# Performance work log

Hardware: AMD Instinct MI355X
Metric: run time of the kernel (lower is better)

Reference implementation:

```python
import jax, jax.numpy as jnp
import numpy as np

E = 1024      # embed_dim
H = 16        # num_heads
DH = E // H   # head_dim
CD = 512      # context_dim
S = 2048      # source length
B = 16        # batch
SCALE = DH ** -0.5


def setup_inputs() -> dict:
    key0 = jax.random.key(0)
    ks = jax.random.split(key0, 12)
    inp = {
        "query": jax.random.normal(ks[0], (1, B, E), jnp.float32),
        "key": jax.random.normal(ks[1], (S, B, E), jnp.float32),
        "value": jax.random.normal(ks[2], (S, B, E), jnp.float32),
        "context": jax.random.normal(ks[3], (B, CD), jnp.float32),
        # packed QKV input projection: [3E, E] (rows 0:E -> Q, E:2E -> K, 2E:3E -> V)
        "in_proj_weight": jax.random.normal(ks[4], (3 * E, E), jnp.float32) * 0.02,
        "in_proj_bias": jnp.zeros((3 * E,), jnp.float32),
        # context_layer: Linear(context_dim + embed_dim, embed_dim)
        "ctx_weight": jax.random.normal(ks[5], (E, CD + E), jnp.float32) * 0.02,
        "ctx_bias": jnp.zeros((E,), jnp.float32),
        # out_proj: Linear(E, E)
        "out_weight": jax.random.normal(ks[6], (E, E), jnp.float32) * 0.02,
        "out_bias": jnp.zeros((E,), jnp.float32),
        # bias_k / bias_v: learned extra KV position, shape [1,1,E] in torch
        "bias_k": jax.random.normal(ks[7], (E,), jnp.float32) * 0.02,
        "bias_v": jax.random.normal(ks[8], (E,), jnp.float32) * 0.02,
    }
    return inp


def _attention(query, key, value, context, in_proj_weight, in_proj_bias,
               ctx_weight, ctx_bias, out_weight, out_bias, bias_k, bias_v):
    tgt_len, bsz, _ = query.shape  # tgt_len == 1 (context cat requires it)
    # separate q/k/v input projections (slices of packed weight)
    q = query @ in_proj_weight[:E].T + in_proj_bias[:E]
    k = key @ in_proj_weight[E:2 * E].T + in_proj_bias[E:2 * E]
    v = value @ in_proj_weight[2 * E:].T + in_proj_bias[2 * E:]
    # context injection: concat context along feature dim, project back to E
    ctx_q = context[None]                                # [1, B, CD]
    ctx_k = jnp.broadcast_to(context[None], (k.shape[0], bsz, CD))
    q = jnp.concatenate([ctx_q, q], axis=-1) @ ctx_weight.T + ctx_bias
    k = jnp.concatenate([ctx_k, k], axis=-1) @ ctx_weight.T + ctx_bias
    q = q * SCALE
    # bias_k / bias_v appended as extra source position
    k = jnp.concatenate([k, jnp.broadcast_to(bias_k, (1, bsz, E))], axis=0)
    v = jnp.concatenate([v, jnp.broadcast_to(bias_v, (1, bsz, E))], axis=0)
    src_len = k.shape[0]
    # [L, B, E] -> [B*H, L, DH]
    qh = q.reshape(tgt_len, bsz * H, DH).transpose(1, 0, 2)
    kh = k.reshape(src_len, bsz * H, DH).transpose(1, 0, 2)
    vh = v.reshape(src_len, bsz * H, DH).transpose(1, 0, 2)
    scores = jnp.einsum("btd,bsd->bts", qh, kh)          # [B*H, T, S+1]
    weights = jax.nn.softmax(scores, axis=-1)
    attn = jnp.einsum("bts,bsd->btd", weights, vh)       # [B*H, T, DH]
    attn = attn.transpose(1, 0, 2).reshape(tgt_len, bsz, E)
    attn = attn @ out_weight.T + out_bias
    avg_weights = weights.reshape(bsz, H, tgt_len, src_len).sum(axis=1) / H
    return attn, avg_weights


def reference(query, key, value, context, in_proj_weight, in_proj_bias,
              ctx_weight, ctx_bias, out_weight, out_bias, bias_k, bias_v):
    return _attention(query, key, value, context, in_proj_weight, in_proj_bias,
                      ctx_weight, ctx_bias, out_weight, out_bias, bias_k, bias_v)
```

## Files before the change

### kernel.cpp

```cpp
#include <hip/hip_runtime.h>
#include <math.h>

#define E   1024
#define H   16
#define DH  64
#define CD  512
#define S   2048
#define B   16
#define SRC (S + 1)
#define SPAD 2052
#define SCALE 0.125f

#define OFF_CTXP 0
#define OFF_Q0   16384
#define OFF_BKP  32768
#define OFF_Q1S  33792
#define OFF_CK   50176
#define OFF_TT   66560
#define OFF_GP   328960
#define OFF_SC   1377536
#define OFF_WT   1902848
#define OFF_UP   2427392
#define OFF_U    10816000
#define OFF_AP   11078144

__global__ __launch_bounds__(256) void k_pre1(
    const float* __restrict__ query, const float* __restrict__ context,
    const float* __restrict__ ipw, const float* __restrict__ ipb,
    const float* __restrict__ cw, const float* __restrict__ cb,
    float* __restrict__ ws)
{
    int b  = blockIdx.x >> 6;
    int et = blockIdx.x & 63;
    int grp = threadIdx.x >> 4, l = threadIdx.x & 15;
    int e = et * 16 + grp;
    const float* crow = cw + (size_t)e * (CD + E);
    const float* ctx  = context + b * CD;
    float a1 = 0.f;
    #pragma unroll
    for (int c = l * 4; c < CD; c += 64) {
        float4 w4 = *(const float4*)(crow + c);
        float4 x4 = *(const float4*)(ctx + c);
        a1 += w4.x*x4.x + w4.y*x4.y + w4.z*x4.z + w4.w*x4.w;
    }
    const float* qrow = query + b * E;
    const float* wrow = ipw + (size_t)e * E;
    float a2 = 0.f;
    #pragma unroll
    for (int f = l * 4; f < E; f += 64) {
        float4 w4 = *(const float4*)(wrow + f);
        float4 x4 = *(const float4*)(qrow + f);
        a2 += w4.x*x4.x + w4.y*x4.y + w4.z*x4.z + w4.w*x4.w;
    }
    float a3 = 0.f;
    if (b == 0) {
        const float* c2 = crow + CD;
        const float* bk = ipb + E;
        #pragma unroll
        for (int f = l * 4; f < E; f += 64) {
            float4 w4 = *(const float4*)(c2 + f);
            float4 x4 = *(const float4*)(bk + f);
            a3 += w4.x*x4.x + w4.y*x4.y + w4.z*x4.z + w4.w*x4.w;
        }
    }
    #pragma unroll
    for (int m = 8; m >= 1; m >>= 1) {
        a1 += __shfl_xor(a1, m, 64);
        a2 += __shfl_xor(a2, m, 64);
        a3 += __shfl_xor(a3, m, 64);
    }
    if (l == 0) {
        ws[OFF_CTXP + b*E + e] = a1 + cb[e];
        ws[OFF_Q0   + b*E + e] = a2 + ipb[e];
        if (b == 0) ws[OFF_BKP + e] = a3;
    }
}

__global__ __launch_bounds__(256) void k_pre2(
    const float* __restrict__ cw, float* __restrict__ ws)
{
    int b  = blockIdx.x >> 6;
    int et = blockIdx.x & 63;
    int grp = threadIdx.x >> 4, l = threadIdx.x & 15;
    int e = et * 16 + grp;
    const float* q0 = ws + OFF_Q0 + b*E;
    const float* c2row = cw + (size_t)e * (CD + E) + CD;
    float acc = 0.f;
    #pragma unroll
    for (int f = l * 4; f < E; f += 64) {
        float4 w4 = *(const float4*)(c2row + f);
        float4 x4 = *(const float4*)(q0 + f);
        acc += w4.x*x4.x + w4.y*x4.y + w4.z*x4.z + w4.w*x4.w;
    }
    #pragma unroll
    for (int m = 8; m >= 1; m >>= 1) acc += __shfl_xor(acc, m, 64);
    if (l == 0) {
        float ctxp = ws[OFF_CTXP + b*E + e];
        ws[OFF_Q1S + b*E + e] = (ctxp + acc) * SCALE;
        ws[OFF_CK  + b*E + e] = ctxp + ws[OFF_BKP + e];
    }
}

__global__ __launch_bounds__(256) void k_pre3(
    const float* __restrict__ cw, float* __restrict__ ws)
{
    int bh = blockIdx.x;
    int b = bh >> 4, h = bh & 15;
    int f = threadIdx.x * 4;
    const float* q1 = ws + OFF_Q1S + b*E + h*DH;
    float4 a; a.x = a.y = a.z = a.w = 0.f;
    #pragma unroll 8
    for (int d = 0; d < DH; ++d) {
        float q = q1[d];
        float4 w4 = *(const float4*)(cw + (size_t)(h*DH + d)*(CD+E) + CD + f);
        a.x += q*w4.x; a.y += q*w4.y; a.z += q*w4.z; a.w += q*w4.w;
    }
    *(float4*)(ws + OFF_TT + (size_t)bh*1024 + f) = a;
}

__global__ __launch_bounds__(256) void k_g(
    const float* __restrict__ ipw, float* __restrict__ ws)
{
    int kc = blockIdx.x >> 7;
    int nt = (blockIdx.x >> 5) & 3;
    int mt = blockIdx.x & 31;
    int n  = (nt << 8) + threadIdx.x;
    int m0 = mt << 3;
    int f0 = kc << 8;
    const float* tT = ws + OFF_TT;
    const float* wk = ipw + (size_t)E * E;
    float acc[8];
    #pragma unroll
    for (int m = 0; m < 8; ++m) acc[m] = 0.f;
    #pragma unroll 4
    for (int f = f0; f < f0 + 256; ++f) {
        float wv = wk[(size_t)f*E + n];
        #pragma unroll
        for (int m = 0; m < 8; ++m)
            acc[m] += tT[(size_t)(m0+m)*1024 + f] * wv;
    }
    float* gp = ws + OFF_GP + (size_t)kc * (256*E);
    #pragma unroll
    for (int m = 0; m < 8; ++m) gp[(size_t)(m0+m)*E + n] = acc[m];
}

__global__ __launch_bounds__(256) void k_gsum(float* __restrict__ ws)
{
    int id = blockIdx.x * 256 + threadIdx.x;
    float a = ws[OFF_GP + id]
            + ws[OFF_GP + 1*(256*E) + id]
            + ws[OFF_GP + 2*(256*E) + id]
            + ws[OFF_GP + 3*(256*E) + id];
    ws[OFF_GP + id] = a;
}

__global__ __launch_bounds__(512, 2) void k_scores(
    const float* __restrict__ key, const float* __restrict__ bias_k,
    float* __restrict__ ws)
{
    __shared__ float lds[8704];
    __shared__ float exA[256];
    __shared__ float exB[256];
    int b  = blockIdx.x >> 5;
    int sc = blockIdx.x & 31;
    int tid = threadIdx.x;

    if (tid < 256) {
        int h = tid >> 4, seg = tid & 15;
        const float* q1 = ws + OFF_Q1S + b*E + h*DH + seg*4;
        const float* ck = ws + OFF_CK  + b*E + h*DH + seg*4;
        const float* bk = bias_k + h*DH + seg*4;
        float4 q4 = *(const float4*)q1;
        float4 c4 = *(const float4*)ck;
        float4 b4 = *(const float4*)bk;
        exA[tid] = q4.x*c4.x + q4.y*c4.y + q4.z*c4.z + q4.w*c4.w;
        exB[tid] = q4.x*b4.x + q4.y*b4.y + q4.z*b4.z + q4.w*b4.w;
    }

    int w = __builtin_amdgcn_readfirstlane(tid >> 6);
    int l = tid & 63;
    int r = sc*64 + l;
    const float* kbase = key + (((size_t)r*B + b) << 10) + w*128;
    const float* gbase = ws + OFF_GP + (size_t)b*(16*1024) + w*128;
    float acc[16];
    #pragma unroll
    for (int h = 0; h < 16; ++h) acc[h] = 0.f;

    #pragma unroll 1
    for (int sub = 0; sub < 4; ++sub) {
        const float* kp = kbase + sub*32;
        float4 kk[8];
        #pragma unroll
        for (int j = 0; j < 8; ++j) kk[j] = *(const float4*)(kp + j*4);
        const float* gp0 = gbase + sub*32;
        #pragma unroll
        for (int h = 0; h < 16; ++h) {
            const float* gp = gp0 + h*1024;
            float a = 0.f;
            #pragma unroll
            for (int j = 0; j < 8; ++j) {
                float4 gv = *(const float4*)(gp + j*4);
                a += kk[j].x*gv.x + kk[j].y*gv.y + kk[j].z*gv.z + kk[j].w*gv.w;
            }
            acc[h] += a;
        }
    }

    float* pr = lds + (w*64 + l)*17;
    #pragma unroll
    for (int h = 0; h < 16; ++h) pr[h] = acc[h];
    __syncthreads();

    int l2 = tid & 63, pp = tid >> 6;
    #pragma unroll
    for (int k2 = 0; k2 < 2; ++k2) {
        int h = pp*2 + k2;
        float sum = 0.f;
        #pragma unroll
        for (int ww = 0; ww < 8; ++ww) sum += lds[(ww*64 + l2)*17 + h];
        float c0 = 0.f;
        #pragma unroll
        for (int seg = 0; seg < 16; ++seg) c0 += exA[h*16 + seg];
        int bh = b*16 + h;
        ws[OFF_SC + (size_t)bh*SPAD + sc*64 + l2] = sum + c0;
        if (sc == 0 && l2 == 0) {
            float sb = 0.f;
            #pragma unroll
            for (int seg = 0; seg < 16; ++seg) sb += exB[h*16 + seg];
            ws[OFF_SC + (size_t)bh*SPAD + S] = sb;
        }
    }
}

__global__ __launch_bounds__(256) void k_softmax(float* __restrict__ ws)
{
    int bh = blockIdx.x;
    int tid = threadIdx.x, lane = tid & 63, wid = tid >> 6;
    const float* row = ws + OFF_SC + (size_t)bh*SPAD;
    __shared__ float red[4];
    float v[9];
    float m = -1e30f;
    #pragma unroll
    for (int i = 0; i < 9; ++i) {
        int s = tid + (i << 8);
        if (s < SRC) { v[i] = row[s]; m = fmaxf(m, v[i]); } else v[i] = -1e30f;
    }
    #pragma unroll
    for (int k = 1; k < 64; k <<= 1) m = fmaxf(m, __shfl_xor(m, k, 64));
    if (lane == 0) red[wid] = m;
    __syncthreads();
    m = fmaxf(fmaxf(red[0], red[1]), fmaxf(red[2], red[3]));
    __syncthreads();
    float sum = 0.f;
    #pragma unroll
    for (int i = 0; i < 9; ++i) {
        int s = tid + (i << 8);
        if (s < SRC) { v[i] = expf(v[i] - m); sum += v[i]; }
    }
    #pragma unroll
    for (int k = 1; k < 64; k <<= 1) sum += __shfl_xor(sum, k, 64);
    if (lane == 0) red[wid] = sum;
    __syncthreads();
    sum = red[0] + red[1] + red[2] + red[3];
    float inv = 1.0f / sum;
    float* wrow = ws + OFF_WT + (size_t)bh*SRC;
    #pragma unroll
    for (int i = 0; i < 9; ++i) {
        int s = tid + (i << 8);
        if (s < SRC) wrow[s] = v[i] * inv;
    }
}

__global__ __launch_bounds__(256) void k_avg(
    const float* __restrict__ ws, float* __restrict__ out)
{
    int b = blockIdx.x / 9, i = blockIdx.x % 9;
    int s = i*256 + threadIdx.x;
    if (s >= SRC) return;
    const float* p = ws + OFF_WT + (size_t)(b*16)*SRC + s;
    float a = 0.f;
    #pragma unroll
    for (int h = 0; h < 16; ++h) a += p[(size_t)h*SRC];
    out[B*E + b*SRC + s] = a * (1.0f / H);
}

__global__ __launch_bounds__(256) void k_u(
    const float* __restrict__ value, float* __restrict__ ws)
{
    int b  = blockIdx.x >> 5;
    int sc = blockIdx.x & 31;
    int f  = threadIdx.x * 4;
    const float* wtb = ws + OFF_WT + (size_t)(b*16)*SRC;
    float4 acc[16];
    #pragma unroll
    for (int h = 0; h < 16; ++h) { acc[h].x = acc[h].y = acc[h].z = acc[h].w = 0.f; }
    int s0 = sc * 64;
    #pragma unroll 1
    for (int sub = 0; sub < 8; ++sub) {
        int ss = s0 + sub*8;
        float4 vv[8];
        #pragma unroll
        for (int j = 0; j < 8; ++j)
            vv[j] = *(const float4*)(value + (((size_t)(ss+j)*B + b) << 10) + f);
        #pragma unroll
        for (int h = 0; h < 16; ++h) {
            const float* wr = wtb + (size_t)h*SRC + ss;
            #pragma unroll
            for (int j = 0; j < 8; ++j) {
                float wv = wr[j];
                acc[h].x += wv*vv[j].x; acc[h].y += wv*vv[j].y;
                acc[h].z += wv*vv[j].z; acc[h].w += wv*vv[j].w;
            }
        }
    }
    float* up = ws + OFF_UP + ((size_t)(sc*B + b)*16)*1024;
    #pragma unroll
    for (int h = 0; h < 16; ++h)
        *(float4*)(up + (size_t)h*1024 + f) = acc[h];
}

__global__ __launch_bounds__(256) void k_ured(float* __restrict__ ws)
{
    int id = blockIdx.x * 256 + threadIdx.x;
    float4 a; a.x = a.y = a.z = a.w = 0.f;
    #pragma unroll
    for (int c = 0; c < 32; ++c) {
        float4 v = *(const float4*)(ws + OFF_UP + (size_t)c*(B*H*E) + id*4);
        a.x += v.x; a.y += v.y; a.z += v.z; a.w += v.w;
    }
    *(float4*)(ws + OFF_U + id*4) = a;
}

__global__ __launch_bounds__(256) void k_attnpre(
    const float* __restrict__ ipw, const float* __restrict__ ipb,
    const float* __restrict__ bias_v, float* __restrict__ ws)
{
    int b  = blockIdx.x >> 6;
    int et = blockIdx.x & 63;
    int grp = threadIdx.x >> 4, l = threadIdx.x & 15;
    int e = et * 16 + grp;
    int h = e >> 6;
    const float* wvr = ipw + (size_t)(2*E + e) * E;
    const float* ur  = ws + OFF_U + (size_t)(b*16 + h) * E;
    float acc = 0.f;
    #pragma unroll
    for (int ff = l * 4; ff < E; ff += 64) {
        float4 w4 = *(const float4*)(wvr + ff);
        float4 u4 = *(const float4*)(ur + ff);
        acc += w4.x*u4.x + w4.y*u4.y + w4.z*u4.z + w4.w*u4.w;
    }
    #pragma unroll
    for (int m = 8; m >= 1; m >>= 1) acc += __shfl_xor(acc, m, 64);
    if (l == 0) {
        float wS = ws[OFF_WT + (size_t)(b*16 + h)*SRC + S];
        ws[OFF_AP + b*E + e] = acc + ipb[2*E + e] * (1.0f - wS) + wS * bias_v[e];
    }
}

__global__ __launch_bounds__(256) void k_out(
    const float* __restrict__ ow, const float* __restrict__ ob,
    const float* __restrict__ ws, float* __restrict__ out)
{
    int b  = blockIdx.x >> 6;
    int et = blockIdx.x & 63;
    int grp = threadIdx.x >> 4, l = threadIdx.x & 15;
    int o = et * 16 + grp;
    const float* wr = ow + (size_t)o * E;
    const float* ap = ws + OFF_AP + b*E;
    float acc = 0.f;
    #pragma unroll
    for (int e = l * 4; e < E; e += 64) {
        float4 w4 = *(const float4*)(wr + e);
        float4 a4 = *(const float4*)(ap + e);
        acc += w4.x*a4.x + w4.y*a4.y + w4.z*a4.z + w4.w*a4.w;
    }
    #pragma unroll
    for (int m = 8; m >= 1; m >>= 1) acc += __shfl_xor(acc, m, 64);
    if (l == 0) out[b*E + o] = acc + ob[o];
}

extern "C" void kernel_launch(void* const* d_in, const int* in_sizes, int n_in,
                              void* d_out, int out_size, void* d_ws, size_t ws_size,
                              hipStream_t stream)
{
    const float* query   = (const float*)d_in[0];
    const float* key     = (const float*)d_in[1];
    const float* value   = (const float*)d_in[2];
    const float* context = (const float*)d_in[3];
    const float* ipw     = (const float*)d_in[4];
    const float* ipb     = (const float*)d_in[5];
    const float* cw      = (const float*)d_in[6];
    const float* cb      = (const float*)d_in[7];
    const float* ow      = (const float*)d_in[8];
    const float* ob      = (const float*)d_in[9];
    const float* bias_k  = (const float*)d_in[10];
    const float* bias_v  = (const float*)d_in[11];
    float* out = (float*)d_out;
    float* ws  = (float*)d_ws;

    hipLaunchKernelGGL(k_pre1,    dim3(1024), dim3(256),  0, stream, query, context, ipw, ipb, cw, cb, ws);
    hipLaunchKernelGGL(k_pre2,    dim3(1024), dim3(256),  0, stream, cw, ws);
    hipLaunchKernelGGL(k_pre3,    dim3(256),  dim3(256),  0, stream, cw, ws);
    hipLaunchKernelGGL(k_g,       dim3(512),  dim3(256),  0, stream, ipw, ws);
    hipLaunchKernelGGL(k_gsum,    dim3(1024), dim3(256),  0, stream, ws);
    hipLaunchKernelGGL(k_scores,  dim3(512),  dim3(512),  0, stream, key, bias_k, ws);
    hipLaunchKernelGGL(k_softmax, dim3(256),  dim3(256),  0, stream, ws);
    hipLaunchKernelGGL(k_avg,     dim3(144),  dim3(256),  0, stream, ws, out);
    hipLaunchKernelGGL(k_u,       dim3(512),  dim3(256),  0, stream, value, ws);
    hipLaunchKernelGGL(k_ured,    dim3(256),  dim3(256),  0, stream, ws);
    hipLaunchKernelGGL(k_attnpre, dim3(1024), dim3(256),  0, stream, ipw, ipb, bias_v, ws);
    hipLaunchKernelGGL(k_out,     dim3(1024), dim3(256),  0, stream, ow, ob, ws, out);
}
```

Before: 183.7 us.

## Reuse projection weights across batch in small GEMV kernels, retile G GEMM

```diff
diff --git a/kernel.cpp b/kernel.cpp
--- a/kernel.cpp
+++ b/kernel.cpp
@@ -30,128 +30,146 @@
     const float* __restrict__ cw, const float* __restrict__ cb,
     float* __restrict__ ws)
 {
-    int b  = blockIdx.x >> 6;
-    int et = blockIdx.x & 63;
+    int et = blockIdx.x;
     int grp = threadIdx.x >> 4, l = threadIdx.x & 15;
     int e = et * 16 + grp;
     const float* crow = cw + (size_t)e * (CD + E);
-    const float* ctx  = context + b * CD;
-    float a1 = 0.f;
-    #pragma unroll
-    for (int c = l * 4; c < CD; c += 64) {
-        float4 w4 = *(const float4*)(crow + c);
-        float4 x4 = *(const float4*)(ctx + c);
-        a1 += w4.x*x4.x + w4.y*x4.y + w4.z*x4.z + w4.w*x4.w;
-    }
-    const float* qrow = query + b * E;
     const float* wrow = ipw + (size_t)e * E;
-    float a2 = 0.f;
-    #pragma unroll
-    for (int f = l * 4; f < E; f += 64) {
-        float4 w4 = *(const float4*)(wrow + f);
-        float4 x4 = *(const float4*)(qrow + f);
-        a2 += w4.x*x4.x + w4.y*x4.y + w4.z*x4.z + w4.w*x4.w;
-    }
-    float a3 = 0.f;
-    if (b == 0) {
+    float4 wc[8], wa[16];
+    #pragma unroll
+    for (int j = 0; j < 8; ++j)  wc[j] = *(const float4*)(crow + l*4 + j*64);
+    #pragma unroll
+    for (int j = 0; j < 16; ++j) wa[j] = *(const float4*)(wrow + l*4 + j*64);
+
+    {
         const float* c2 = crow + CD;
         const float* bk = ipb + E;
-        #pragma unroll
-        for (int f = l * 4; f < E; f += 64) {
-            float4 w4 = *(const float4*)(c2 + f);
-            float4 x4 = *(const float4*)(bk + f);
+        float a3 = 0.f;
+        #pragma unroll
+        for (int j = 0; j < 16; ++j) {
+            float4 w4 = *(const float4*)(c2 + l*4 + j*64);
+            float4 x4 = *(const float4*)(bk + l*4 + j*64);
             a3 += w4.x*x4.x + w4.y*x4.y + w4.z*x4.z + w4.w*x4.w;
         }
-    }
-    #pragma unroll
-    for (int m = 8; m >= 1; m >>= 1) {
-        a1 += __shfl_xor(a1, m, 64);
-        a2 += __shfl_xor(a2, m, 64);
-        a3 += __shfl_xor(a3, m, 64);
-    }
-    if (l == 0) {
-        ws[OFF_CTXP + b*E + e] = a1 + cb[e];
-        ws[OFF_Q0   + b*E + e] = a2 + ipb[e];
-        if (b == 0) ws[OFF_BKP + e] = a3;
+        #pragma unroll
+        for (int m = 8; m >= 1; m >>= 1) a3 += __shfl_xor(a3, m, 64);
+        if (l == 0) ws[OFF_BKP + e] = a3;
+    }
+
+    float cbv = cb[e], ibv = ipb[e];
+    #pragma unroll 1
+    for (int b = 0; b < B; ++b) {
+        const float* ctx = context + b * CD;
+        const float* qr  = query   + b * E;
+        float a1 = 0.f, a2 = 0.f;
+        #pragma unroll
+        for (int j = 0; j < 8; ++j) {
+            float4 x4 = *(const float4*)(ctx + l*4 + j*64);
+            a1 += wc[j].x*x4.x + wc[j].y*x4.y + wc[j].z*x4.z + wc[j].w*x4.w;
+        }
+        #pragma unroll
+        for (int j = 0; j < 16; ++j) {
+            float4 x4 = *(const float4*)(qr + l*4 + j*64);
+            a2 += wa[j].x*x4.x + wa[j].y*x4.y + wa[j].z*x4.z + wa[j].w*x4.w;
+        }
+        #pragma unroll
+        for (int m = 8; m >= 1; m >>= 1) {
+            a1 += __shfl_xor(a1, m, 64);
+            a2 += __shfl_xor(a2, m, 64);
+        }
+        if (l == 0) {
+            ws[OFF_CTXP + b*E + e] = a1 + cbv;
+            ws[OFF_Q0   + b*E + e] = a2 + ibv;
+        }
     }
 }
 
 __global__ __launch_bounds__(256) void k_pre2(
     const float* __restrict__ cw, float* __restrict__ ws)
 {
-    int b  = blockIdx.x >> 6;
-    int et = blockIdx.x & 63;
+    int et = blockIdx.x;
     int grp = threadIdx.x >> 4, l = threadIdx.x & 15;
     int e = et * 16 + grp;
-    const float* q0 = ws + OFF_Q0 + b*E;
     const float* c2row = cw + (size_t)e * (CD + E) + CD;
-    float acc = 0.f;
-    #pragma unroll
-    for (int f = l * 4; f < E; f += 64) {
-        float4 w4 = *(const float4*)(c2row + f);
-        float4 x4 = *(const float4*)(q0 + f);
-        acc += w4.x*x4.x + w4.y*x4.y + w4.z*x4.z + w4.w*x4.w;
-    }
-    #pragma unroll
-    for (int m = 8; m >= 1; m >>= 1) acc += __shfl_xor(acc, m, 64);
-    if (l == 0) {
-        float ctxp = ws[OFF_CTXP + b*E + e];
-        ws[OFF_Q1S + b*E + e] = (ctxp + acc) * SCALE;
-        ws[OFF_CK  + b*E + e] = ctxp + ws[OFF_BKP + e];
+    float4 wz[16];
+    #pragma unroll
+    for (int j = 0; j < 16; ++j) wz[j] = *(const float4*)(c2row + l*4 + j*64);
+
+    #pragma unroll 1
+    for (int b = 0; b < B; ++b) {
+        const float* q0 = ws + OFF_Q0 + b*E;
+        float acc = 0.f;
+        #pragma unroll
+        for (int j = 0; j < 16; ++j) {
+            float4 x4 = *(const float4*)(q0 + l*4 + j*64);
+            acc += wz[j].x*x4.x + wz[j].y*x4.y + wz[j].z*x4.z + wz[j].w*x4.w;
+        }
+        #pragma unroll
+        for (int m = 8; m >= 1; m >>= 1) acc += __shfl_xor(acc, m, 64);
+        if (l == 0) {
+            float ctxp = ws[OFF_CTXP + b*E + e];
+            ws[OFF_Q1S + b*E + e] = (ctxp + acc) * SCALE;
+        }
     }
 }
 
 __global__ __launch_bounds__(256) void k_pre3(
     const float* __restrict__ cw, float* __restrict__ ws)
 {
-    int bh = blockIdx.x;
-    int b = bh >> 4, h = bh & 15;
-    int f = threadIdx.x * 4;
-    const float* q1 = ws + OFF_Q1S + b*E + h*DH;
-    float4 a; a.x = a.y = a.z = a.w = 0.f;
-    #pragma unroll 8
+    int h  = blockIdx.x >> 2;
+    int ft = blockIdx.x & 3;
+    int f  = ft*256 + threadIdx.x;
+    float acc[16];
+    #pragma unroll
+    for (int b = 0; b < 16; ++b) acc[b] = 0.f;
+    #pragma unroll 4
     for (int d = 0; d < DH; ++d) {
-        float q = q1[d];
-        float4 w4 = *(const float4*)(cw + (size_t)(h*DH + d)*(CD+E) + CD + f);
-        a.x += q*w4.x; a.y += q*w4.y; a.z += q*w4.z; a.w += q*w4.w;
-    }
-    *(float4*)(ws + OFF_TT + (size_t)bh*1024 + f) = a;
+        float w = cw[(size_t)(h*DH + d)*(CD+E) + CD + f];
+        #pragma unroll
+        for (int b = 0; b < 16; ++b)
+            acc[b] += ws[OFF_Q1S + b*E + h*DH + d] * w;
+    }
+    #pragma unroll
+    for (int b = 0; b < 16; ++b)
+        ws[OFF_TT + (size_t)(b*16 + h)*1024 + f] = acc[b];
 }
 
 __global__ __launch_bounds__(256) void k_g(
     const float* __restrict__ ipw, float* __restrict__ ws)
 {
-    int kc = blockIdx.x >> 7;
-    int nt = (blockIdx.x >> 5) & 3;
-    int mt = blockIdx.x & 31;
-    int n  = (nt << 8) + threadIdx.x;
-    int m0 = mt << 3;
-    int f0 = kc << 8;
+    int kc = blockIdx.x >> 6;
+    int nt = (blockIdx.x >> 4) & 3;
+    int mt = blockIdx.x & 15;
+    int n  = nt*256 + threadIdx.x;
+    int m0 = mt*16;
+    int f0 = kc*256;
     const float* tT = ws + OFF_TT;
     const float* wk = ipw + (size_t)E * E;
-    float acc[8];
-    #pragma unroll
-    for (int m = 0; m < 8; ++m) acc[m] = 0.f;
+    float acc[16];
+    #pragma unroll
+    for (int m = 0; m < 16; ++m) acc[m] = 0.f;
     #pragma unroll 4
     for (int f = f0; f < f0 + 256; ++f) {
         float wv = wk[(size_t)f*E + n];
         #pragma unroll
-        for (int m = 0; m < 8; ++m)
+        for (int m = 0; m < 16; ++m)
             acc[m] += tT[(size_t)(m0+m)*1024 + f] * wv;
     }
     float* gp = ws + OFF_GP + (size_t)kc * (256*E);
     #pragma unroll
-    for (int m = 0; m < 8; ++m) gp[(size_t)(m0+m)*E + n] = acc[m];
+    for (int m = 0; m < 16; ++m) gp[(size_t)(m0+m)*E + n] = acc[m];
 }
 
 __global__ __launch_bounds__(256) void k_gsum(float* __restrict__ ws)
 {
     int id = blockIdx.x * 256 + threadIdx.x;
-    float a = ws[OFF_GP + id]
-            + ws[OFF_GP + 1*(256*E) + id]
-            + ws[OFF_GP + 2*(256*E) + id]
-            + ws[OFF_GP + 3*(256*E) + id];
-    ws[OFF_GP + id] = a;
+    float4 a; a.x = a.y = a.z = a.w = 0.f;
+    #pragma unroll
+    for (int c = 0; c < 4; ++c) {
+        float4 v = *(const float4*)(ws + OFF_GP + (size_t)c*(256*E) + id*4);
+        a.x += v.x; a.y += v.y; a.z += v.z; a.w += v.w;
+    }
+    *(float4*)(ws + OFF_GP + id*4) = a;
 }
 
 __global__ __launch_bounds__(512, 2) void k_scores(
@@ -168,12 +186,15 @@
     if (tid < 256) {
         int h = tid >> 4, seg = tid & 15;
         const float* q1 = ws + OFF_Q1S + b*E + h*DH + seg*4;
-        const float* ck = ws + OFF_CK  + b*E + h*DH + seg*4;
+        const float* cp = ws + OFF_CTXP + b*E + h*DH + seg*4;
+        const float* bp = ws + OFF_BKP + h*DH + seg*4;
         const float* bk = bias_k + h*DH + seg*4;
         float4 q4 = *(const float4*)q1;
-        float4 c4 = *(const float4*)ck;
+        float4 c4 = *(const float4*)cp;
+        float4 p4 = *(const float4*)bp;
         float4 b4 = *(const float4*)bk;
-        exA[tid] = q4.x*c4.x + q4.y*c4.y + q4.z*c4.z + q4.w*c4.w;
+        exA[tid] = q4.x*(c4.x+p4.x) + q4.y*(c4.y+p4.y)
+                 + q4.z*(c4.z+p4.z) + q4.w*(c4.w+p4.w);
         exB[tid] = q4.x*b4.x + q4.y*b4.y + q4.z*b4.z + q4.w*b4.w;
     }
 
@@ -335,25 +356,30 @@
     const float* __restrict__ ipw, const float* __restrict__ ipb,
     const float* __restrict__ bias_v, float* __restrict__ ws)
 {
-    int b  = blockIdx.x >> 6;
-    int et = blockIdx.x & 63;
+    int et = blockIdx.x;
     int grp = threadIdx.x >> 4, l = threadIdx.x & 15;
     int e = et * 16 + grp;
     int h = e >> 6;
     const float* wvr = ipw + (size_t)(2*E + e) * E;
-    const float* ur  = ws + OFF_U + (size_t)(b*16 + h) * E;
-    float acc = 0.f;
-    #pragma unroll
-    for (int ff = l * 4; ff < E; ff += 64) {
-        float4 w4 = *(const float4*)(wvr + ff);
-        float4 u4 = *(const float4*)(ur + ff);
-        acc += w4.x*u4.x + w4.y*u4.y + w4.z*u4.z + w4.w*u4.w;
-    }
-    #pragma unroll
-    for (int m = 8; m >= 1; m >>= 1) acc += __shfl_xor(acc, m, 64);
-    if (l == 0) {
-        float wS = ws[OFF_WT + (size_t)(b*16 + h)*SRC + S];
-        ws[OFF_AP + b*E + e] = acc + ipb[2*E + e] * (1.0f - wS) + wS * bias_v[e];
+    float4 wv[16];
+    #pragma unroll
+    for (int i = 0; i < 16; ++i) wv[i] = *(const float4*)(wvr + l*4 + i*64);
+    float bv = ipb[2*E + e], bvv = bias_v[e];
+    #pragma unroll 1
+    for (int b = 0; b < B; ++b) {
+        const float* ur = ws + OFF_U + (size_t)(b*16 + h) * E;
+        float acc = 0.f;
+        #pragma unroll
+        for (int i = 0; i < 16; ++i) {
+            float4 u4 = *(const float4*)(ur + l*4 + i*64);
+            acc += wv[i].x*u4.x + wv[i].y*u4.y + wv[i].z*u4.z + wv[i].w*u4.w;
+        }
+        #pragma unroll
+        for (int m = 8; m >= 1; m >>= 1) acc += __shfl_xor(acc, m, 64);
+        if (l == 0) {
+            float wS = ws[OFF_WT + (size_t)(b*16 + h)*SRC + S];
+            ws[OFF_AP + b*E + e] = acc + bv * (1.0f - wS) + wS * bvv;
+        }
     }
 }
 
@@ -361,22 +387,27 @@
     const float* __restrict__ ow, const float* __restrict__ ob,
     const float* __restrict__ ws, float* __restrict__ out)
 {
-    int b  = blockIdx.x >> 6;
-    int et = blockIdx.x & 63;
+    int et = blockIdx.x;
     int grp = threadIdx.x >> 4, l = threadIdx.x & 15;
     int o = et * 16 + grp;
     const float* wr = ow + (size_t)o * E;
-    const float* ap = ws + OFF_AP + b*E;
-    float acc = 0.f;
-    #pragma unroll
-    for (int e = l * 4; e < E; e += 64) {
-        float4 w4 = *(const float4*)(wr + e);
-        float4 a4 = *(const float4*)(ap + e);
-        acc += w4.x*a4.x + w4.y*a4.y + w4.z*a4.z + w4.w*a4.w;
-    }
-    #pragma unroll
-    for (int m = 8; m >= 1; m >>= 1) acc += __shfl_xor(acc, m, 64);
-    if (l == 0) out[b*E + o] = acc + ob[o];
+    float4 wvv[16];
+    #pragma unroll
+    for (int i = 0; i < 16; ++i) wvv[i] = *(const float4*)(wr + l*4 + i*64);
+    float obv = ob[o];
+    #pragma unroll 1
+    for (int b = 0; b < B; ++b) {
+        const float* ap = ws + OFF_AP + b*E;
+        float acc = 0.f;
+        #pragma unroll
+        for (int i = 0; i < 16; ++i) {
+            float4 a4 = *(const float4*)(ap + l*4 + i*64);
+            acc += wvv[i].x*a4.x + wvv[i].y*a4.y + wvv[i].z*a4.z + wvv[i].w*a4.w;
+        }
+        #pragma unroll
+        for (int m = 8; m >= 1; m >>= 1) acc += __shfl_xor(acc, m, 64);
+        if (l == 0) out[b*E + o] = acc + obv;
+    }
 }
 
 extern "C" void kernel_launch(void* const* d_in, const int* in_sizes, int n_in,
@@ -398,16 +429,16 @@
     float* out = (float*)d_out;
     float* ws  = (float*)d_ws;
 
-    hipLaunchKernelGGL(k_pre1,    dim3(1024), dim3(256),  0, stream, query, context, ipw, ipb, cw, cb, ws);
-    hipLaunchKernelGGL(k_pre2,    dim3(1024), dim3(256),  0, stream, cw, ws);
-    hipLaunchKernelGGL(k_pre3,    dim3(256),  dim3(256),  0, stream, cw, ws);
-    hipLaunchKernelGGL(k_g,       dim3(512),  dim3(256),  0, stream, ipw, ws);
-    hipLaunchKernelGGL(k_gsum,    dim3(1024), dim3(256),  0, stream, ws);
+    hipLaunchKernelGGL(k_pre1,    dim3(64),   dim3(256),  0, stream, query, context, ipw, ipb, cw, cb, ws);
+    hipLaunchKernelGGL(k_pre2,    dim3(64),   dim3(256),  0, stream, cw, ws);
+    hipLaunchKernelGGL(k_pre3,    dim3(64),   dim3(256),  0, stream, cw, ws);
+    hipLaunchKernelGGL(k_g,       dim3(256),  dim3(256),  0, stream, ipw, ws);
+    hipLaunchKernelGGL(k_gsum,    dim3(256),  dim3(256),  0, stream, ws);
     hipLaunchKernelGGL(k_scores,  dim3(512),  dim3(512),  0, stream, key, bias_k, ws);
     hipLaunchKernelGGL(k_softmax, dim3(256),  dim3(256),  0, stream, ws);
     hipLaunchKernelGGL(k_avg,     dim3(144),  dim3(256),  0, stream, ws, out);
     hipLaunchKernelGGL(k_u,       dim3(512),  dim3(256),  0, stream, value, ws);
     hipLaunchKernelGGL(k_ured,    dim3(256),  dim3(256),  0, stream, ws);
-    hipLaunchKernelGGL(k_attnpre, dim3(1024), dim3(256),  0, stream, ipw, ipb, bias_v, ws);
-    hipLaunchKernelGGL(k_out,     dim3(1024), dim3(256),  0, stream, ow, ob, ws, out);
-}
+    hipLaunchKernelGGL(k_attnpre, dim3(64),   dim3(256),  0, stream, ipw, ipb, bias_v, ws);
+    hipLaunchKernelGGL(k_out,     dim3(64),   dim3(256),  0, stream, ow, ob, ws, out);
+}
```

After: 417.4 us. 2.27x slower.
